# Kernel tuning notes

Measured on AMD Instinct MI355X. Metric: run time of the kernel, lower is better.

Reference implementation:

```python
import jax, jax.numpy as jnp
import numpy as np
from jax import lax

N = 64          # padded / uniform graph size
B = 512         # number of graph pairs
E = 512         # edges per graph
GCN_SIZES = [64, 32, 16]
CONV_OUT = [8, 16, 32]
D_IN = 16


def gcn_conv(x, src, dst, W, b):
    # PyG GCNConv: add self-loops, symmetric norm D^-1/2 (A+I) D^-1/2, then XW + b
    n = x.shape[0]
    h = x @ W
    deg = jnp.zeros((n,), x.dtype).at[dst].add(1.0) + 1.0  # +1 self-loop
    dinv = lax.rsqrt(deg)
    msg = h[src] * (dinv[src] * dinv[dst])[:, None]
    agg = jnp.zeros_like(h).at[dst].add(msg) + h * (dinv * dinv)[:, None]
    return agg + b


def gcn_pass(x, ei, Ws, bs):
    src, dst = ei[0], ei[1]
    feats = []
    h = x
    for i in range(len(Ws)):
        h = gcn_conv(h, src, dst, Ws[i], bs[i])
        feats.append(h)               # pre-ReLU features are used for similarity
        if i < len(Ws) - 1:
            h = jax.nn.relu(h)        # dropout p used in eval -> identity
    return feats


def conv_same(x, w, b):
    y = lax.conv_general_dilated(x, w, (1, 1), 'SAME',
                                 dimension_numbers=('NCHW', 'OIHW', 'NCHW'))
    return y + b[None, :, None, None]


def maxpool2(x):
    return lax.reduce_window(x, -jnp.inf, lax.max, (1, 1, 2, 2), (1, 1, 2, 2), 'VALID')


def setup_inputs() -> dict:
    key = jax.random.key(0)
    ks = jax.random.split(key, 32)
    f32 = jnp.float32
    x_q = jax.random.normal(ks[0], (B * N, D_IN), f32)
    x_c = jax.random.normal(ks[1], (B * N, D_IN), f32)
    off = (jnp.arange(B, dtype=jnp.int32) * N)[:, None]
    eq_s = (jax.random.randint(ks[2], (B, E), 0, N, jnp.int32) + off).reshape(-1)
    eq_d = (jax.random.randint(ks[3], (B, E), 0, N, jnp.int32) + off).reshape(-1)
    ec_s = (jax.random.randint(ks[4], (B, E), 0, N, jnp.int32) + off).reshape(-1)
    ec_d = (jax.random.randint(ks[5], (B, E), 0, N, jnp.int32) + off).reshape(-1)
    edge_q = jnp.stack([eq_s, eq_d])
    edge_c = jnp.stack([ec_s, ec_d])

    def lin(k, fi, fo):
        return jax.random.normal(k, (fi, fo), f32) / np.sqrt(fi)

    inp = dict(x_q=x_q, x_c=x_c, edge_q=edge_q, edge_c=edge_c)
    dims = [D_IN] + GCN_SIZES
    for i in range(3):
        inp[f'gcn_w{i+1}'] = lin(ks[6 + i], dims[i], dims[i + 1])
        inp[f'gcn_b{i+1}'] = jnp.zeros((dims[i + 1],), f32)
    cin = [1] + CONV_OUT[:-1]
    for i in range(3):
        fan = cin[i] * 25
        inp[f'conv_w{i+1}'] = jax.random.normal(ks[10 + i], (3, CONV_OUT[i], cin[i], 5, 5), f32) / np.sqrt(fan)
        inp[f'conv_b{i+1}'] = jnp.zeros((3, CONV_OUT[i]), f32)
    inp['lin_w1'] = lin(ks[14], 6144, 256)
    inp['lin_b1'] = jnp.zeros((256,), f32)
    inp['lin_w2'] = lin(ks[15], 256, 16)
    inp['lin_b2'] = jnp.zeros((16,), f32)
    inp['score_w'] = lin(ks[16], 16, 1)
    inp['score_b'] = jnp.zeros((1,), f32)
    return inp


def _forward(x_q, x_c, gcn_w1, gcn_b1, gcn_w2, gcn_b2, gcn_w3, gcn_b3,
             conv_w1, conv_b1, conv_w2, conv_b2, conv_w3, conv_b3,
             lin_w1, lin_b1, lin_w2, lin_b2, score_w, score_b,
             edge_q, edge_c):
    Ws = (gcn_w1, gcn_w2, gcn_w3)
    bs = (gcn_b1, gcn_b2, gcn_b3)
    qf = gcn_pass(x_q, edge_q, Ws, bs)   # list of [B*N, d_i]
    cf = gcn_pass(x_c, edge_c, Ws, bs)
    sims = [jnp.einsum('bnd,bmd->bnm', q.reshape(B, N, -1), c.reshape(B, N, -1))
            for q, c in zip(qf, cf)]
    cw = (conv_w1, conv_w2, conv_w3)
    cb = (conv_b1, conv_b2, conv_b3)
    outs = []
    for m in range(3):                    # separate conv weights per similarity matrix
        z = sims[m][:, None]              # [B, 1, N, N]
        for l in range(3):
            z = maxpool2(jax.nn.relu(conv_same(z, cw[l][m], cb[l][m])))
        outs.append(z)                    # [B, 32, 8, 8]
    feat = jnp.concatenate(outs, axis=1).reshape(B, 6144)
    h = jax.nn.relu(feat @ lin_w1 + lin_b1)
    h = jax.nn.relu(h @ lin_w2 + lin_b2)
    return (h @ score_w + score_b).reshape(-1)  # is_sig=False -> logits [B]


def reference(x_q, x_c, edge_q, edge_c, gcn_w1, gcn_b1, gcn_w2, gcn_b2, gcn_w3, gcn_b3,
              conv_w1, conv_b1, conv_w2, conv_b2, conv_w3, conv_b3,
              lin_w1, lin_b1, lin_w2, lin_b2, score_w, score_b):
    return _forward(x_q, x_c, gcn_w1, gcn_b1, gcn_w2, gcn_b2, gcn_w3, gcn_b3,
                    conv_w1, conv_b1, conv_w2, conv_b2, conv_w3, conv_b3,
                    lin_w1, lin_b1, lin_w2, lin_b2, score_w, score_b,
                    edge_q, edge_c)
```

## Files before the change

kernel.cpp:

```cpp
#include <hip/hip_runtime.h>
#include <hip/hip_bf16.h>

constexpr int B = 512, N = 64, E = 512, NE = B * E;

typedef __attribute__((ext_vector_type(8))) short bf8v;
typedef __attribute__((ext_vector_type(4))) float f32x4;
typedef unsigned short u16;

__device__ __forceinline__ u16 f2bf(float f) {
  unsigned u = __builtin_bit_cast(unsigned, f);
  u += 0x7FFFu + ((u >> 16) & 1u);
  return (u16)(u >> 16);
}

__device__ __forceinline__ int cmin(int a, int b) { return a < b ? a : b; }

template <int DIN, int DOUT, bool STORE_NEXT>
__device__ __forceinline__ void gcn_layer(
    float* __restrict__ At, float* __restrict__ Xt, float* __restrict__ Hs,
    float* __restrict__ Wls, const float* __restrict__ W,
    const float* __restrict__ bias, u16* __restrict__ fout, int g, int t) {
  constexpr int XS = 68;
  for (int i = t; i < DIN * DOUT; i += 512) Wls[i] = W[i];
  __syncthreads();
  constexpr int CT = DOUT / 2;
  const int ct = t % CT, nt = t / CT;
  if (nt < 16) {
    float acc[4][2] = {};
#pragma unroll 4
    for (int k = 0; k < DIN; ++k) {
      float4 xv = *(const float4*)&Xt[k * XS + 4 * nt];
      float2 wv = *(const float2*)&Wls[k * DOUT + 2 * ct];
      float xa[4] = {xv.x, xv.y, xv.z, xv.w};
#pragma unroll
      for (int i = 0; i < 4; ++i) {
        acc[i][0] += xa[i] * wv.x;
        acc[i][1] += xa[i] * wv.y;
      }
    }
#pragma unroll
    for (int i = 0; i < 4; ++i)
      *(float2*)&Hs[(4 * nt + i) * XS + 2 * ct] = make_float2(acc[i][0], acc[i][1]);
  }
  __syncthreads();
  if (nt < 16) {
    float acc[4][2] = {};
#pragma unroll 4
    for (int s = 0; s < N; ++s) {
      float4 av = *(const float4*)&At[s * XS + 4 * nt];
      float2 hv = *(const float2*)&Hs[s * XS + 2 * ct];
      float aa[4] = {av.x, av.y, av.z, av.w};
#pragma unroll
      for (int i = 0; i < 4; ++i) {
        acc[i][0] += aa[i] * hv.x;
        acc[i][1] += aa[i] * hv.y;
      }
    }
    const float2 bv = *(const float2*)&bias[2 * ct];
#pragma unroll
    for (int i = 0; i < 4; ++i) {
      float2 st = make_float2(acc[i][0] + bv.x, acc[i][1] + bv.y);
      unsigned pack = (unsigned)f2bf(st.x) | ((unsigned)f2bf(st.y) << 16);
      *(unsigned*)&fout[(size_t)g * N * DOUT + (size_t)(4 * nt + i) * DOUT + 2 * ct] = pack;
      if (STORE_NEXT) {
        Xt[(2 * ct + 0) * XS + 4 * nt + i] = fmaxf(st.x, 0.f);
        Xt[(2 * ct + 1) * XS + 4 * nt + i] = fmaxf(st.y, 0.f);
      }
    }
  }
  __syncthreads();
}

__global__ __launch_bounds__(512) void gcn_fused(
    const float* __restrict__ xq, const float* __restrict__ xc,
    const float* __restrict__ W1, const float* __restrict__ b1,
    const float* __restrict__ W2, const float* __restrict__ b2,
    const float* __restrict__ W3, const float* __restrict__ b3,
    const int* __restrict__ eq, const int* __restrict__ ec,
    u16* __restrict__ f1q, u16* __restrict__ f1c,
    u16* __restrict__ f2q, u16* __restrict__ f2c,
    u16* __restrict__ f3q, u16* __restrict__ f3c) {
  constexpr int XS = 68;
  __shared__ __align__(16) float At[N * XS];
  __shared__ __align__(16) float Xt[N * XS];
  __shared__ __align__(16) float Hs[N * XS];
  __shared__ __align__(16) float Wls[64 * 32];
  __shared__ float dl[N];
  __shared__ int cnt[N];
  const int g = blockIdx.x, t = threadIdx.x;
  const float* x = blockIdx.y ? xc : xq;
  const int* edges = blockIdx.y ? ec : eq;
  u16* o1 = blockIdx.y ? f1c : f1q;
  u16* o2 = blockIdx.y ? f2c : f2q;
  u16* o3 = blockIdx.y ? f3c : f3q;
  for (int i = t; i < N * 16; i += 512) {
    int n = i / 16, k = i % 16;
    Xt[k * XS + n] = x[(size_t)g * N * 16 + i];
  }
  for (int i = t; i < N * XS; i += 512) At[i] = 0.f;
  if (t < N) cnt[t] = 1;
  __syncthreads();
  const int* srcp = edges + (size_t)g * E;
  const int* dstp = edges + NE + (size_t)g * E;
  for (int j = t; j < E; j += 512) atomicAdd(&cnt[dstp[j] & 63], 1);
  __syncthreads();
  if (t < N) dl[t] = rsqrtf((float)cnt[t]);
  __syncthreads();
  for (int j = t; j < E; j += 512) {
    int s = srcp[j] & 63, d = dstp[j] & 63;
    atomicAdd(&At[s * XS + d], dl[s] * dl[d]);
  }
  if (t < N) atomicAdd(&At[t * XS + t], dl[t] * dl[t]);
  __syncthreads();
  gcn_layer<16, 64, true>(At, Xt, Hs, Wls, W1, b1, o1, g, t);
  gcn_layer<64, 32, true>(At, Xt, Hs, Wls, W2, b2, o2, g, t);
  gcn_layer<32, 16, false>(At, Xt, Hs, Wls, W3, b3, o3, g, t);
}

__global__ __launch_bounds__(256, 4) void simconv1(
    const u16* __restrict__ f1q, const u16* __restrict__ f1c,
    const u16* __restrict__ f2q, const u16* __restrict__ f2c,
    const u16* __restrict__ f3q, const u16* __restrict__ f3c,
    const float* __restrict__ w, const float* __restrict__ bias,
    u16* __restrict__ out) {
  constexpr int PS = 68, QS = 72;
  __shared__ __align__(16) u16 Qs[64 * QS];
  __shared__ __align__(16) u16 Cs[64 * QS];
  __shared__ __align__(16) float simp[68 * 68];
  __shared__ float wls[25 * 8];
  __shared__ float bls[8];
  const int b = blockIdx.x, m = blockIdx.y, t = threadIdx.x;
  for (int i = t; i < 68 * 68; i += 256) simp[i] = 0.f;
  if (t < 200) {
    int oc = t / 25, tap = t % 25;
    wls[tap * 8 + oc] = w[m * 200 + t];
  }
  if (t < 8) bls[t] = bias[m * 8 + t];
  const u16* fq = (m == 0) ? f1q : (m == 1) ? f2q : f3q;
  const u16* fc = (m == 0) ? f1c : (m == 1) ? f2c : f3c;
  const int D = 64 >> m;
  const int SEG = D >> 3;
  for (int i = t; i < 64 * SEG; i += 256) {
    int n = i / SEG, s = i - n * SEG;
    *(uint4*)&Qs[n * QS + s * 8] = *(const uint4*)&fq[(size_t)b * 64 * D + n * D + s * 8];
    *(uint4*)&Cs[n * QS + s * 8] = *(const uint4*)&fc[(size_t)b * 64 * D + n * D + s * 8];
  }
  if (m == 2 && t < 128) {
    int n = t >> 1, s = t & 1;
    uint4 z = {0u, 0u, 0u, 0u};
    *(uint4*)&Qs[n * QS + 16 + s * 8] = z;
    *(uint4*)&Cs[n * QS + 16 + s * 8] = z;
  }
  __syncthreads();
  const int w4 = t >> 6, lane = t & 63;
  const int r16 = lane & 15, kg = lane >> 4;
  const int Kpad = (m == 0) ? 64 : 32;
#pragma unroll 1
  for (int ct = 0; ct < 4; ++ct) {
    f32x4 acc = {0.f, 0.f, 0.f, 0.f};
    for (int ks = 0; ks < Kpad; ks += 32) {
      bf8v a = *(const bf8v*)&Qs[(w4 * 16 + r16) * QS + ks + kg * 8];
      bf8v bb = *(const bf8v*)&Cs[(ct * 16 + r16) * QS + ks + kg * 8];
      acc = __builtin_amdgcn_mfma_f32_16x16x32_bf16(a, bb, acc, 0, 0, 0);
    }
#pragma unroll
    for (int j = 0; j < 4; ++j)
      simp[(w4 * 16 + kg * 4 + j + 2) * PS + ct * 16 + r16 + 2] = acc[j];
  }
  __syncthreads();
  const int gy = t >> 4, gx = t & 15;
  float pr[8][8];
#pragma unroll
  for (int yy = 0; yy < 8; ++yy) {
    float4 a = *(const float4*)&simp[(4 * gy + yy) * PS + 4 * gx];
    float4 bb = *(const float4*)&simp[(4 * gy + yy) * PS + 4 * gx + 4];
    pr[yy][0] = a.x; pr[yy][1] = a.y; pr[yy][2] = a.z; pr[yy][3] = a.w;
    pr[yy][4] = bb.x; pr[yy][5] = bb.y; pr[yy][6] = bb.z; pr[yy][7] = bb.w;
  }
  u16* op = out + (size_t)(b * 3 + m) * 8192;
#pragma unroll 1
  for (int p2 = 0; p2 < 4; ++p2) {
    float acc[2][16];
#pragma unroll
    for (int p = 0; p < 16; ++p) { acc[0][p] = 0.f; acc[1][p] = 0.f; }
#pragma unroll
    for (int ky = 0; ky < 5; ++ky)
#pragma unroll
      for (int kx = 0; kx < 5; ++kx) {
        float2 wv = *(const float2*)&wls[(ky * 5 + kx) * 8 + p2 * 2];
#pragma unroll
        for (int dy = 0; dy < 4; ++dy)
#pragma unroll
          for (int dx = 0; dx < 4; ++dx) {
            float rv = pr[ky + dy][kx + dx];
            acc[0][dy * 4 + dx] += rv * wv.x;
            acc[1][dy * 4 + dx] += rv * wv.y;
          }
      }
    float b0 = bls[p2 * 2], b1 = bls[p2 * 2 + 1];
#pragma unroll
    for (int ay = 0; ay < 2; ++ay)
#pragma unroll
      for (int ax = 0; ax < 2; ++ax) {
        float v0 = fmaxf(fmaxf(acc[0][(2 * ay) * 4 + 2 * ax], acc[0][(2 * ay) * 4 + 2 * ax + 1]),
                         fmaxf(acc[0][(2 * ay + 1) * 4 + 2 * ax], acc[0][(2 * ay + 1) * 4 + 2 * ax + 1]));
        float v1 = fmaxf(fmaxf(acc[1][(2 * ay) * 4 + 2 * ax], acc[1][(2 * ay) * 4 + 2 * ax + 1]),
                         fmaxf(acc[1][(2 * ay + 1) * 4 + 2 * ax], acc[1][(2 * ay + 1) * 4 + 2 * ax + 1]));
        v0 = fmaxf(v0 + b0, 0.f);
        v1 = fmaxf(v1 + b1, 0.f);
        unsigned pack = (unsigned)f2bf(v0) | ((unsigned)f2bf(v1) << 16);
        *(unsigned*)&op[(size_t)(((2 * gy + ay) * 32) + (2 * gx + ax)) * 8 + p2 * 2] = pack;
      }
  }
}

__global__ __launch_bounds__(256) void wprep_kernel(const float* __restrict__ cw2,
                                                    const float* __restrict__ cw3,
                                                    u16* __restrict__ w2p,
                                                    u16* __restrict__ w3p) {
  int i = blockIdx.x * 256 + threadIdx.x;
  if (i < 3 * 7 * 16 * 40) {
    int m = i / 4480, r = i % 4480;
    int k = r % 40, rest = r / 40, oc = rest & 15, st = rest >> 4;
    u16 v = 0;
    if (k < 32) {
      int sl = k >> 3, ci = k & 7, tap = st * 4 + sl;
      if (tap < 25) v = f2bf(cw2[((size_t)(m * 16 + oc) * 8 + ci) * 25 + tap]);
    }
    w2p[i] = v;
  }
  if (i < 3 * 26 * 16 * 40) {
    int m = i / 16640, r = i % 16640;
    int k = r % 40, rest = r / 40, oc16 = rest & 15, sthalf = rest >> 4;
    int half = sthalf & 1, st = sthalf >> 1;
    u16 v = 0;
    if (k < 32) {
      int sl = k >> 4, ci = k & 15, tap = st * 2 + sl;
      int oc = half * 16 + oc16;
      if (tap < 25) v = f2bf(cw3[((size_t)(m * 32 + oc) * 16 + ci) * 25 + tap]);
    }
    w3p[i] = v;
  }
}

__global__ __launch_bounds__(256) void conv2_mfma(
    const u16* __restrict__ in, const u16* __restrict__ w2p,
    const float* __restrict__ bias, u16* __restrict__ out) {
  constexpr int PW = 36, BS = 40;
  __shared__ __align__(16) u16 ins[PW * PW * 8];
  __shared__ __align__(16) u16 wls[7 * 16 * BS];
  __shared__ float bls[16];
  const int b = blockIdx.x, m = blockIdx.y, t = threadIdx.x;
  const size_t ibase = (size_t)(b * 3 + m) * 8192;
  for (int i = t; i < PW * PW; i += 256) {
    int y = i / PW, x = i % PW;
    uint4 v = {0u, 0u, 0u, 0u};
    if (y >= 2 && y < 34 && x >= 2 && x < 34)
      v = *(const uint4*)&in[ibase + (size_t)((y - 2) * 32 + (x - 2)) * 8];
    *(uint4*)&ins[i * 8] = v;
  }
  {
    const u16* wsrc = w2p + m * 4480;
    for (int i = t; i < 560; i += 256) *(uint4*)&wls[i * 8] = *(const uint4*)&wsrc[i * 8];
  }
  if (t < 16) bls[t] = bias[m * 16 + t];
  __syncthreads();
  const int wv = t >> 6, lane = t & 63;
  const int oc = lane & 15, g = lane >> 4;
  const int xt = wv & 1, ypb = wv >> 1;
  const int x = xt * 16 + oc;
  const size_t obase = (size_t)(b * 3 + m) * 4096;
#pragma unroll 1
  for (int grp = 0; grp < 2; ++grp) {
    f32x4 acc[4][2];
#pragma unroll
    for (int i = 0; i < 4; ++i) {
      acc[i][0] = (f32x4){0.f, 0.f, 0.f, 0.f};
      acc[i][1] = (f32x4){0.f, 0.f, 0.f, 0.f};
    }
#pragma unroll
    for (int st = 0; st < 7; ++st) {
      bf8v bvv = *(const bf8v*)&wls[(st * 16 + oc) * BS + g * 8];
      const int c0 = cmin(st * 4 + 0, 24), c1 = cmin(st * 4 + 1, 24);
      const int c2 = cmin(st * 4 + 2, 24), c3 = cmin(st * 4 + 3, 24);
      const int k0 = (c0 / 5) * PW + c0 % 5, k1 = (c1 / 5) * PW + c1 % 5;
      const int k2 = (c2 / 5) * PW + c2 % 5, k3 = (c3 / 5) * PW + c3 % 5;
      const int koff = (g == 0) ? k0 : (g == 1) ? k1 : (g == 2) ? k2 : k3;
#pragma unroll
      for (int i = 0; i < 4; ++i) {
        const int y0 = 2 * ypb + 4 * (grp * 4 + i);
        const int abase = (y0 * PW + x + koff) * 8;
        bf8v a0 = *(const bf8v*)&ins[abase];
        acc[i][0] = __builtin_amdgcn_mfma_f32_16x16x32_bf16(a0, bvv, acc[i][0], 0, 0, 0);
        bf8v a1 = *(const bf8v*)&ins[abase + PW * 8];
        acc[i][1] = __builtin_amdgcn_mfma_f32_16x16x32_bf16(a1, bvv, acc[i][1], 0, 0, 0);
      }
    }
    const float bb = bls[oc];
#pragma unroll
    for (int i = 0; i < 4; ++i) {
      const int yp = ypb + 2 * (grp * 4 + i);
      const float v0 = fmaxf(fmaxf(fmaxf(acc[i][0][0], acc[i][0][1]),
                                   fmaxf(acc[i][1][0], acc[i][1][1])) + bb, 0.f);
      const float v1 = fmaxf(fmaxf(fmaxf(acc[i][0][2], acc[i][0][3]),
                                   fmaxf(acc[i][1][2], acc[i][1][3])) + bb, 0.f);
      const int px = xt * 8 + 2 * g;
      out[obase + (size_t)((yp * 16 + px) * 16 + oc)] = f2bf(v0);
      out[obase + (size_t)((yp * 16 + px + 1) * 16 + oc)] = f2bf(v1);
    }
  }
}

__global__ __launch_bounds__(256) void conv3_mfma(
    const u16* __restrict__ in, const u16* __restrict__ w3p,
    const float* __restrict__ bias, u16* __restrict__ feat) {
  constexpr int PW = 20, BS = 40;
  __shared__ __align__(16) u16 ins[PW * PW * 16];
  __shared__ __align__(16) u16 wls[26 * 16 * BS];
  __shared__ float bls[32];
  const int b = blockIdx.x, m = blockIdx.y, t = threadIdx.x;
  const size_t ibase = (size_t)(b * 3 + m) * 4096;
  for (int i = t; i < PW * PW; i += 256) {
    int y = i / PW, x = i % PW;
    uint4 v0 = {0u, 0u, 0u, 0u}, v1 = {0u, 0u, 0u, 0u};
    if (y >= 2 && y < 18 && x >= 2 && x < 18) {
      const u16* p = &in[ibase + (size_t)((y - 2) * 16 + (x - 2)) * 16];
      v0 = *(const uint4*)p;
      v1 = *(const uint4*)(p + 8);
    }
    *(uint4*)&ins[i * 16] = v0;
    *(uint4*)&ins[i * 16 + 8] = v1;
  }
  {
    const u16* wsrc = w3p + m * 16640;
    for (int i = t; i < 2080; i += 256) *(uint4*)&wls[i * 8] = *(const uint4*)&wsrc[i * 8];
  }
  if (t < 32) bls[t] = bias[m * 32 + t];
  __syncthreads();
  const int wv = t >> 6, lane = t & 63;
  const int oc = lane & 15, g = lane >> 4;
  const int sl = g >> 1, ch = (g & 1) * 8;
  const int half = wv & 1, ypb = wv >> 1;
  u16* fb = feat + (size_t)b * 6144 + m * 2048;
  f32x4 acc[4][2];
#pragma unroll
  for (int i = 0; i < 4; ++i) {
    acc[i][0] = (f32x4){0.f, 0.f, 0.f, 0.f};
    acc[i][1] = (f32x4){0.f, 0.f, 0.f, 0.f};
  }
#pragma unroll
  for (int st = 0; st < 13; ++st) {
    bf8v bvv = *(const bf8v*)&wls[(size_t)((st * 2 + half) * 16 + oc) * BS + g * 8];
    const int c0 = cmin(st * 2 + 0, 24), c1 = cmin(st * 2 + 1, 24);
    const int k0 = (c0 / 5) * PW + c0 % 5, k1 = (c1 / 5) * PW + c1 % 5;
    const int koff = sl ? k1 : k0;
#pragma unroll
    for (int i = 0; i < 4; ++i) {
      const int y0 = 2 * ypb + 4 * i;
      const int abase = (y0 * PW + oc + koff) * 16 + ch;
      bf8v a0 = *(const bf8v*)&ins[abase];
      acc[i][0] = __builtin_amdgcn_mfma_f32_16x16x32_bf16(a0, bvv, acc[i][0], 0, 0, 0);
      bf8v a1 = *(const bf8v*)&ins[abase + PW * 16];
      acc[i][1] = __builtin_amdgcn_mfma_f32_16x16x32_bf16(a1, bvv, acc[i][1], 0, 0, 0);
    }
  }
  const int ocg = half * 16 + oc;
  const float bb = bls[ocg];
#pragma unroll
  for (int i = 0; i < 4; ++i) {
    const int yp = ypb + 2 * i;
    const float v0 = fmaxf(fmaxf(fmaxf(acc[i][0][0], acc[i][0][1]),
                                 fmaxf(acc[i][1][0], acc[i][1][1])) + bb, 0.f);
    const float v1 = fmaxf(fmaxf(fmaxf(acc[i][0][2], acc[i][0][3]),
                                 fmaxf(acc[i][1][2], acc[i][1][3])) + bb, 0.f);
    unsigned pack = (unsigned)f2bf(v0) | ((unsigned)f2bf(v1) << 16);
    *(unsigned*)&fb[ocg * 64 + yp * 8 + 2 * g] = pack;
  }
}

__global__ __launch_bounds__(256) void wcvt_kernel(const float* __restrict__ W,
                                                   u16* __restrict__ wT) {
  __shared__ float tile[64][65];
  const int k0 = blockIdx.x * 64, c0 = blockIdx.y * 64, t = threadIdx.x;
  for (int i = t; i < 4096; i += 256) {
    int r = i >> 6, c = i & 63;
    tile[r][c] = W[(size_t)(k0 + r) * 256 + c0 + c];
  }
  __syncthreads();
  for (int i = t; i < 4096; i += 256) {
    int c = i >> 6, k = i & 63;
    wT[(size_t)(c0 + c) * 6144 + k0 + k] = f2bf(tile[k][c]);
  }
}

__global__ __launch_bounds__(256) void lin1_mfma(const u16* __restrict__ feat,
                                                 const u16* __restrict__ wT,
                                                 float* __restrict__ h1p) {
  constexpr int AS = 72;
  __shared__ __align__(16) u16 As[64 * AS];
  __shared__ __align__(16) u16 Bs[64 * AS];
  const int r0 = blockIdx.x * 64, c0 = blockIdx.y * 64, kb = blockIdx.z * 384;
  const int t = threadIdx.x;
  const int w = t >> 6, lane = t & 63;
  const int row16 = lane & 15, kg = lane >> 4;
  f32x4 acc[4] = {{0.f, 0.f, 0.f, 0.f}, {0.f, 0.f, 0.f, 0.f},
                  {0.f, 0.f, 0.f, 0.f}, {0.f, 0.f, 0.f, 0.f}};
  const int lr = t >> 2, lk = (t & 3) * 16;
#pragma unroll 1
  for (int st = 0; st < 6; ++st) {
    __syncthreads();
    const int ks = kb + st * 64;
    {
      const u16* srcA = feat + (size_t)(r0 + lr) * 6144 + ks + lk;
      uint4 a0 = *(const uint4*)srcA;
      uint4 a1 = *(const uint4*)(srcA + 8);
      *(uint4*)&As[lr * AS + lk] = a0;
      *(uint4*)&As[lr * AS + lk + 8] = a1;
      const u16* srcB = wT + (size_t)(c0 + lr) * 6144 + ks + lk;
      uint4 b0 = *(const uint4*)srcB;
      uint4 b1 = *(const uint4*)(srcB + 8);
      *(uint4*)&Bs[lr * AS + lk] = b0;
      *(uint4*)&Bs[lr * AS + lk + 8] = b1;
    }
    __syncthreads();
#pragma unroll
    for (int kk = 0; kk < 2; ++kk) {
      bf8v a = *(const bf8v*)&As[(w * 16 + row16) * AS + kk * 32 + kg * 8];
#pragma unroll
      for (int ct = 0; ct < 4; ++ct) {
        bf8v bb = *(const bf8v*)&Bs[(ct * 16 + row16) * AS + kk * 32 + kg * 8];
        acc[ct] = __builtin_amdgcn_mfma_f32_16x16x32_bf16(a, bb, acc[ct], 0, 0, 0);
      }
    }
  }
  float* out = h1p + (size_t)blockIdx.z * 131072;
#pragma unroll
  for (int ct = 0; ct < 4; ++ct)
#pragma unroll
    for (int j = 0; j < 4; ++j)
      out[(size_t)(r0 + w * 16 + kg * 4 + j) * 256 + c0 + ct * 16 + row16] = acc[ct][j];
}

__global__ __launch_bounds__(256) void head_kernel(
    const float* __restrict__ h1p, const float* __restrict__ b1,
    const float* __restrict__ w2, const float* __restrict__ b2,
    const float* __restrict__ sw, const float* __restrict__ sb,
    float* __restrict__ out) {
  constexpr int HS = 260;
  __shared__ __align__(16) float h1s[16 * HS];
  __shared__ __align__(16) float w2s[256 * 16];
  const int r0 = blockIdx.x * 16, t = threadIdx.x;
  for (int i = t; i < 4096; i += 256) {
    int r = i >> 8, k = i & 255;
    float s = b1[k];
#pragma unroll
    for (int p = 0; p < 16; ++p) s += h1p[(size_t)p * 131072 + (size_t)(r0 + r) * 256 + k];
    h1s[r * HS + k] = s;
    w2s[i] = w2[i];
  }
  __syncthreads();
  const int j = t & 15, r = t >> 4;
  float acc = b2[j];
#pragma unroll 4
  for (int k4 = 0; k4 < 64; ++k4) {
    float4 hv = *(const float4*)&h1s[r * HS + 4 * k4];
    float h0 = fmaxf(hv.x, 0.f), h1v = fmaxf(hv.y, 0.f);
    float h2v = fmaxf(hv.z, 0.f), h3 = fmaxf(hv.w, 0.f);
    acc += h0 * w2s[(4 * k4 + 0) * 16 + j];
    acc += h1v * w2s[(4 * k4 + 1) * 16 + j];
    acc += h2v * w2s[(4 * k4 + 2) * 16 + j];
    acc += h3 * w2s[(4 * k4 + 3) * 16 + j];
  }
  float v = fmaxf(acc, 0.f) * sw[j];
#pragma unroll
  for (int off = 8; off; off >>= 1) v += __shfl_xor(v, off, 16);
  if (j == 0) out[r0 + r] = v + sb[0];
}

extern "C" void kernel_launch(void* const* d_in, const int* in_sizes, int n_in,
                              void* d_out, int out_size, void* d_ws, size_t ws_size,
                              hipStream_t stream) {
  const float* x_q = (const float*)d_in[0];
  const float* x_c = (const float*)d_in[1];
  const int* edge_q = (const int*)d_in[2];
  const int* edge_c = (const int*)d_in[3];
  const float* gw1 = (const float*)d_in[4];
  const float* gb1 = (const float*)d_in[5];
  const float* gw2 = (const float*)d_in[6];
  const float* gb2 = (const float*)d_in[7];
  const float* gw3 = (const float*)d_in[8];
  const float* gb3 = (const float*)d_in[9];
  const float* cw1 = (const float*)d_in[10];
  const float* cb1 = (const float*)d_in[11];
  const float* cw2 = (const float*)d_in[12];
  const float* cb2 = (const float*)d_in[13];
  const float* cw3 = (const float*)d_in[14];
  const float* cb3 = (const float*)d_in[15];
  const float* lw1 = (const float*)d_in[16];
  const float* lb1 = (const float*)d_in[17];
  const float* lw2 = (const float*)d_in[18];
  const float* lb2 = (const float*)d_in[19];
  const float* swt = (const float*)d_in[20];
  const float* sbs = (const float*)d_in[21];
  float* ws = (float*)d_ws;

  const size_t o_f1q = 65536;
  const size_t o_f2q = o_f1q + 2097152;
  const size_t o_f3q = o_f2q + 1048576;
  const size_t o_f1c = o_f3q + 524288;
  const size_t o_f2c = o_f1c + 2097152;
  const size_t o_f3c = o_f2c + 1048576;
  const size_t o_sims = o_f3c + 524288;
  const size_t o_pm1 = o_sims + 6291456;
  const size_t o_pm2 = o_pm1 + 6291456;
  const size_t o_wT = o_pm2 + 3145728;
  const size_t o_w2p = o_wT + 786432;
  const size_t o_w3p = o_w2p + 8192;
  const size_t o_feat = o_sims;
  const size_t o_h1p = o_f1q;

  u16* f1q = (u16*)(ws + o_f1q); u16* f2q = (u16*)(ws + o_f2q); u16* f3q = (u16*)(ws + o_f3q);
  u16* f1c = (u16*)(ws + o_f1c); u16* f2c = (u16*)(ws + o_f2c); u16* f3c = (u16*)(ws + o_f3c);
  u16* pm1 = (u16*)(ws + o_pm1);
  u16* pm2 = (u16*)(ws + o_pm2);
  u16* wT = (u16*)(ws + o_wT);
  u16* w2p = (u16*)(ws + o_w2p);
  u16* w3p = (u16*)(ws + o_w3p);
  u16* feat = (u16*)(ws + o_feat);
  float* h1p = ws + o_h1p;

  wcvt_kernel<<<dim3(96, 4), 256, 0, stream>>>(lw1, wT);
  wprep_kernel<<<196, 256, 0, stream>>>(cw2, cw3, w2p, w3p);

  gcn_fused<<<dim3(B, 2), 512, 0, stream>>>(x_q, x_c, gw1, gb1, gw2, gb2, gw3, gb3,
                                            edge_q, edge_c, f1q, f1c, f2q, f2c, f3q, f3c);

  simconv1<<<dim3(B, 3), 256, 0, stream>>>(f1q, f1c, f2q, f2c, f3q, f3c, cw1, cb1, pm1);

  conv2_mfma<<<dim3(B, 3), 256, 0, stream>>>(pm1, w2p, cb2, pm2);
  conv3_mfma<<<dim3(B, 3), 256, 0, stream>>>(pm2, w3p, cb3, feat);

  lin1_mfma<<<dim3(8, 4, 16), 256, 0, stream>>>(feat, wT, h1p);
  head_kernel<<<32, 256, 0, stream>>>(h1p, lb1, lw2, lb2, swt, sbs, (float*)d_out);
}
```

Before: 138.3 us.

## Use all GCN threads, read weights from global, merge weight-prep kernels

Re-parameterizes the GCN layer thread mapping so every one of the 512 threads computes an NR x NC output tile, instead of only the first 16 row-groups being active. Weights are now read directly from global memory rather than staged in shared memory, which removes a copy loop and a barrier per layer and shrinks shared memory use. The two weight preparation kernels are merged into a single launch to save launch overhead. Smaller per-thread tiles reduce register reuse and global weight reads may hit cache less efficiently.

```diff
diff --git a/kernel.cpp b/kernel.cpp
--- a/kernel.cpp
+++ b/kernel.cpp
@@ -15,56 +15,91 @@
 
 __device__ __forceinline__ int cmin(int a, int b) { return a < b ? a : b; }
 
-template <int DIN, int DOUT, bool STORE_NEXT>
+template <int DIN, int DOUT, int NR, int NC, bool STORE_NEXT>
 __device__ __forceinline__ void gcn_layer(
     float* __restrict__ At, float* __restrict__ Xt, float* __restrict__ Hs,
-    float* __restrict__ Wls, const float* __restrict__ W,
-    const float* __restrict__ bias, u16* __restrict__ fout, int g, int t) {
+    const float* __restrict__ W, const float* __restrict__ bias,
+    u16* __restrict__ fout, int g, int t) {
   constexpr int XS = 68;
-  for (int i = t; i < DIN * DOUT; i += 512) Wls[i] = W[i];
-  __syncthreads();
-  constexpr int CT = DOUT / 2;
+  constexpr int CT = DOUT / NC;
+  static_assert((64 / NR) * CT == 512, "thread mapping");
   const int ct = t % CT, nt = t / CT;
-  if (nt < 16) {
-    float acc[4][2] = {};
+  const int n0 = NR * nt, c0 = NC * ct;
+  {
+    float acc[NR][NC] = {};
 #pragma unroll 4
     for (int k = 0; k < DIN; ++k) {
-      float4 xv = *(const float4*)&Xt[k * XS + 4 * nt];
-      float2 wv = *(const float2*)&Wls[k * DOUT + 2 * ct];
-      float xa[4] = {xv.x, xv.y, xv.z, xv.w};
-#pragma unroll
-      for (int i = 0; i < 4; ++i) {
-        acc[i][0] += xa[i] * wv.x;
-        acc[i][1] += xa[i] * wv.y;
-      }
-    }
-#pragma unroll
-    for (int i = 0; i < 4; ++i)
-      *(float2*)&Hs[(4 * nt + i) * XS + 2 * ct] = make_float2(acc[i][0], acc[i][1]);
-  }
-  __syncthreads();
-  if (nt < 16) {
-    float acc[4][2] = {};
+      float xa[NR];
+      if constexpr (NR == 4) {
+        float4 xv = *(const float4*)&Xt[k * XS + n0];
+        xa[0] = xv.x; xa[1] = xv.y; xa[2] = xv.z; xa[3] = xv.w;
+      } else {
+        float2 xv = *(const float2*)&Xt[k * XS + n0];
+        xa[0] = xv.x; xa[1] = xv.y;
+      }
+      float wa[NC];
+      if constexpr (NC == 2) {
+        float2 wv = *(const float2*)&W[k * DOUT + c0];
+        wa[0] = wv.x; wa[1] = wv.y;
+      } else {
+        wa[0] = W[k * DOUT + c0];
+      }
+#pragma unroll
+      for (int i = 0; i < NR; ++i)
+#pragma unroll
+        for (int j = 0; j < NC; ++j) acc[i][j] += xa[i] * wa[j];
+    }
+#pragma unroll
+    for (int i = 0; i < NR; ++i) {
+      if constexpr (NC == 2)
+        *(float2*)&Hs[(n0 + i) * XS + c0] = make_float2(acc[i][0], acc[i][1]);
+      else
+        Hs[(n0 + i) * XS + c0] = acc[i][0];
+    }
+  }
+  __syncthreads();
+  {
+    float acc[NR][NC] = {};
 #pragma unroll 4
     for (int s = 0; s < N; ++s) {
-      float4 av = *(const float4*)&At[s * XS + 4 * nt];
-      float2 hv = *(const float2*)&Hs[s * XS + 2 * ct];
-      float aa[4] = {av.x, av.y, av.z, av.w};
-#pragma unroll
-      for (int i = 0; i < 4; ++i) {
-        acc[i][0] += aa[i] * hv.x;
-        acc[i][1] += aa[i] * hv.y;
-      }
-    }
-    const float2 bv = *(const float2*)&bias[2 * ct];
-#pragma unroll
-    for (int i = 0; i < 4; ++i) {
-      float2 st = make_float2(acc[i][0] + bv.x, acc[i][1] + bv.y);
-      unsigned pack = (unsigned)f2bf(st.x) | ((unsigned)f2bf(st.y) << 16);
-      *(unsigned*)&fout[(size_t)g * N * DOUT + (size_t)(4 * nt + i) * DOUT + 2 * ct] = pack;
+      float aa[NR];
+      if constexpr (NR == 4) {
+        float4 av = *(const float4*)&At[s * XS + n0];
+        aa[0] = av.x; aa[1] = av.y; aa[2] = av.z; aa[3] = av.w;
+      } else {
+        float2 av = *(const float2*)&At[s * XS + n0];
+        aa[0] = av.x; aa[1] = av.y;
+      }
+      float ha[NC];
+      if constexpr (NC == 2) {
+        float2 hv = *(const float2*)&Hs[s * XS + c0];
+        ha[0] = hv.x; ha[1] = hv.y;
+      } else {
+        ha[0] = Hs[s * XS + c0];
+      }
+#pragma unroll
+      for (int i = 0; i < NR; ++i)
+#pragma unroll
+        for (int j = 0; j < NC; ++j) acc[i][j] += aa[i] * ha[j];
+    }
+    float bv[NC];
+#pragma unroll
+    for (int j = 0; j < NC; ++j) bv[j] = bias[c0 + j];
+#pragma unroll
+    for (int i = 0; i < NR; ++i) {
+      float st[NC];
+#pragma unroll
+      for (int j = 0; j < NC; ++j) st[j] = acc[i][j] + bv[j];
+      if constexpr (NC == 2) {
+        unsigned pack = (unsigned)f2bf(st[0]) | ((unsigned)f2bf(st[1]) << 16);
+        *(unsigned*)&fout[(size_t)g * N * DOUT + (size_t)(n0 + i) * DOUT + c0] = pack;
+      } else {
+        fout[(size_t)g * N * DOUT + (size_t)(n0 + i) * DOUT + c0] = f2bf(st[0]);
+      }
       if (STORE_NEXT) {
-        Xt[(2 * ct + 0) * XS + 4 * nt + i] = fmaxf(st.x, 0.f);
-        Xt[(2 * ct + 1) * XS + 4 * nt + i] = fmaxf(st.y, 0.f);
+#pragma unroll
+        for (int j = 0; j < NC; ++j)
+          Xt[(c0 + j) * XS + n0 + i] = fmaxf(st[j], 0.f);
       }
     }
   }
@@ -84,7 +119,6 @@
   __shared__ __align__(16) float At[N * XS];
   __shared__ __align__(16) float Xt[N * XS];
   __shared__ __align__(16) float Hs[N * XS];
-  __shared__ __align__(16) float Wls[64 * 32];
   __shared__ float dl[N];
   __shared__ int cnt[N];
   const int g = blockIdx.x, t = threadIdx.x;
@@ -112,9 +146,9 @@
   }
   if (t < N) atomicAdd(&At[t * XS + t], dl[t] * dl[t]);
   __syncthreads();
-  gcn_layer<16, 64, true>(At, Xt, Hs, Wls, W1, b1, o1, g, t);
-  gcn_layer<64, 32, true>(At, Xt, Hs, Wls, W2, b2, o2, g, t);
-  gcn_layer<32, 16, false>(At, Xt, Hs, Wls, W3, b3, o3, g, t);
+  gcn_layer<16, 64, 4, 2, true>(At, Xt, Hs, W1, b1, o1, g, t);
+  gcn_layer<64, 32, 4, 1, true>(At, Xt, Hs, W2, b2, o2, g, t);
+  gcn_layer<32, 16, 2, 1, false>(At, Xt, Hs, W3, b3, o3, g, t);
 }
 
 __global__ __launch_bounds__(256, 4) void simconv1(
@@ -214,11 +248,26 @@
   }
 }
 
-__global__ __launch_bounds__(256) void wprep_kernel(const float* __restrict__ cw2,
-                                                    const float* __restrict__ cw3,
-                                                    u16* __restrict__ w2p,
-                                                    u16* __restrict__ w3p) {
-  int i = blockIdx.x * 256 + threadIdx.x;
+__global__ __launch_bounds__(256) void prep_kernel(
+    const float* __restrict__ lw1, const float* __restrict__ cw2,
+    const float* __restrict__ cw3, u16* __restrict__ wT,
+    u16* __restrict__ w2p, u16* __restrict__ w3p) {
+  const int t = threadIdx.x;
+  if (blockIdx.x < 384) {
+    __shared__ float tile[64][65];
+    const int k0 = (blockIdx.x % 96) * 64, c0 = (blockIdx.x / 96) * 64;
+    for (int i = t; i < 4096; i += 256) {
+      int r = i >> 6, c = i & 63;
+      tile[r][c] = lw1[(size_t)(k0 + r) * 256 + c0 + c];
+    }
+    __syncthreads();
+    for (int i = t; i < 4096; i += 256) {
+      int c = i >> 6, k = i & 63;
+      wT[(size_t)(c0 + c) * 6144 + k0 + k] = f2bf(tile[k][c]);
+    }
+    return;
+  }
+  int i = (blockIdx.x - 384) * 256 + t;
   if (i < 3 * 7 * 16 * 40) {
     int m = i / 4480, r = i % 4480;
     int k = r % 40, rest = r / 40, oc = rest & 15, st = rest >> 4;
@@ -375,21 +424,6 @@
                                  fmaxf(acc[i][1][2], acc[i][1][3])) + bb, 0.f);
     unsigned pack = (unsigned)f2bf(v0) | ((unsigned)f2bf(v1) << 16);
     *(unsigned*)&fb[ocg * 64 + yp * 8 + 2 * g] = pack;
-  }
-}
-
-__global__ __launch_bounds__(256) void wcvt_kernel(const float* __restrict__ W,
-                                                   u16* __restrict__ wT) {
-  __shared__ float tile[64][65];
-  const int k0 = blockIdx.x * 64, c0 = blockIdx.y * 64, t = threadIdx.x;
-  for (int i = t; i < 4096; i += 256) {
-    int r = i >> 6, c = i & 63;
-    tile[r][c] = W[(size_t)(k0 + r) * 256 + c0 + c];
-  }
-  __syncthreads();
-  for (int i = t; i < 4096; i += 256) {
-    int c = i >> 6, k = i & 63;
-    wT[(size_t)(c0 + c) * 6144 + k0 + k] = f2bf(tile[k][c]);
   }
 }
 
@@ -529,8 +563,7 @@
   u16* feat = (u16*)(ws + o_feat);
   float* h1p = ws + o_h1p;
 
-  wcvt_kernel<<<dim3(96, 4), 256, 0, stream>>>(lw1, wT);
-  wprep_kernel<<<196, 256, 0, stream>>>(cw2, cw3, w2p, w3p);
+  prep_kernel<<<580, 256, 0, stream>>>(lw1, cw2, cw3, wT, w2p, w3p);
 
   gcn_fused<<<dim3(B, 2), 512, 0, stream>>>(x_q, x_c, gw1, gb1, gw2, gb2, gw3, gb3,
                                             edge_q, edge_c, f1q, f1c, f2q, f2c, f3q, f3c);
```

Measured after the change: 136.7 us. About the same (-1.2%).
